# Kernel optimization log

Hardware: AMD Instinct MI355X
Metric: run time of the kernel (lower is better)

The kernel has to match this reference:

```python
import jax, jax.numpy as jnp
import numpy as np

N, C = 2, 256
GH0, GW0 = 40, 40
GH1, GW1 = 40, 40
STRIDE, TOPK = 2, 8
TEMP, THRESH, BORDER = 0.1, 0.2, 2
H0, W0 = GH0 * STRIDE, GW0 * STRIDE
H1, W1 = GH1 * STRIDE, GW1 * STRIDE
K4 = TOPK * STRIDE * STRIDE
# create_meshgrid(2,2) flattened: entries (x, y) in row-major (y outer) order
GRID = jnp.array([[0, 0], [1, 0], [0, 1], [1, 1]], dtype=jnp.int32)


def map_indices(idx, size0, size1):
    # idx: (n, G0, topk) coarse indices into image1 coarse grid
    row = idx[..., None] // size1[1] * STRIDE + GRID[:, 1]
    col = idx[..., None] % size1[1] * STRIDE + GRID[:, 0]
    fine = row * (size1[1] * STRIDE) + col  # (n, G0, topk, 4)
    n = idx.shape[0]
    fine = fine.reshape(n, size0[0], 1, size0[1], 1, -1)
    fine = jnp.broadcast_to(fine, (n, size0[0], STRIDE, size0[1], STRIDE, fine.shape[-1]))
    return fine.reshape(n, size0[0] * size0[1] * STRIDE * STRIDE, -1)


def remove_border_one_side(idx, br, size):
    h, w = size
    pos = jnp.arange(h * w)
    r, c = pos // w, pos % w
    border = (r < br) | (r >= h - br) | (c < br) | (c >= w - br)
    return jnp.where(border[None, :], 0, idx)


def unpatchify(x, grid, stride):
    n, g, s2, c = x.shape
    gh, gw = grid
    x = x.reshape(n, gh, gw, stride, stride, c)
    x = jnp.transpose(x, (0, 5, 1, 3, 2, 4))
    return x.reshape(n, c, gh * stride, gw * stride)


def fused_heatmaps(x0, x1, a01, a10, ind0_f, ind1_f):
    s01 = jnp.einsum('ngqc,ngkc->ngqk', x0, a01) / C  # (n, G0, 4, K4)
    s10 = jnp.einsum('ngqc,ngkc->ngqk', x1, a10) / C
    h01 = jax.nn.softmax(s01 / TEMP, axis=-1)
    h10 = jax.nn.softmax(s10 / TEMP, axis=-1)
    h01 = h01.reshape(N, GH0, GW0, STRIDE, STRIDE, K4)
    h01 = jnp.transpose(h01, (0, 1, 3, 2, 4, 5)).reshape(N, H0 * W0, K4)
    h10 = h10.reshape(N, GH1, GW1, STRIDE, STRIDE, K4)
    h10 = jnp.transpose(h10, (0, 5, 1, 3, 2, 4)).reshape(N, K4, H1 * W1)
    # dense scatter + gather mutual fusion (as in the torch code)
    b = jnp.arange(N)[:, None, None]
    l1 = jnp.arange(H1 * W1)[None, None, :]
    Z0 = jnp.zeros((N, H0 * W0, H1 * W1), h10.dtype).at[b, ind1_f, l1].set(h10)
    new_h01 = h01 * jnp.take_along_axis(Z0, ind0_f, axis=-1)
    l0 = jnp.arange(H0 * W0)[None, :, None]
    Z1 = jnp.zeros((N, H0 * W0, H1 * W1), h01.dtype).at[b, l0, ind0_f].set(h01)
    new_h10 = h10 * jnp.take_along_axis(Z1, ind1_f, axis=-2)
    return new_h01, new_h10


def coarse_matching(h01, h10, ind0_f, ind1_f):
    score = jnp.max(h01, axis=-1)                 # (n, L0)
    sub0 = jnp.argmax(h01, axis=-1)               # (n, L0)
    j_best = jnp.take_along_axis(ind0_f, sub0[..., None], axis=-1)[..., 0]
    sub1 = jnp.argmax(h10, axis=-2)               # (n, L1)
    i_best = jnp.take_along_axis(ind1_f, sub1[:, None, :], axis=-2)[:, 0, :]
    j_best = remove_border_one_side(j_best, BORDER, (H1, W1))
    i_best = remove_border_one_side(i_best, BORDER, (H0, W0))
    biproj = jnp.take_along_axis(i_best, j_best, axis=-1)
    mask = biproj == jnp.arange(H0 * W0)[None, :]
    mask = mask.at[:, 0].set(False)
    mask = mask & (score > THRESH)
    scores = jnp.where(mask, score, 0.0)
    return mask, j_best, scores


def setup_inputs() -> dict:
    key = jax.random.key(0)
    ks = jax.random.split(key, 6)
    return {
        'x0': jax.random.normal(ks[0], (N, GH0 * GW0, 4, C), jnp.float32),
        'x1': jax.random.normal(ks[1], (N, GH1 * GW1, 4, C), jnp.float32),
        'attended0_to_1': jax.random.normal(ks[2], (N, GH0 * GW0, K4, C), jnp.float32),
        'attended1_to_0': jax.random.normal(ks[3], (N, GH1 * GW1, K4, C), jnp.float32),
        'x0_prior': jax.random.normal(ks[4], (N, C, GH0, GW0), jnp.float32),
        'x1_prior': jax.random.normal(ks[5], (N, C, GH1, GW1), jnp.float32),
    }


def reference(x0, x1, attended0_to_1, attended1_to_0, x0_prior, x1_prior):
    p0 = x0_prior.reshape(N, C, GH0 * GW0)
    p1 = x1_prior.reshape(N, C, GH1 * GW1)
    sim = jnp.einsum('nci,ncj->nij', p0, p1) / C  # (n, G0, G1)
    _, i01 = jax.lax.top_k(sim, TOPK)                              # (n, G0, topk)
    _, i10 = jax.lax.top_k(jnp.swapaxes(sim, -2, -1), TOPK)        # (n, G1, topk)
    ind0_f = map_indices(i01, (GH0, GW0), (GH1, GW1))              # (n, L0, K4)
    ind1_f = jnp.swapaxes(map_indices(i10, (GH1, GW1), (GH0, GW0)), -2, -1)  # (n, K4, L1)
    h01, h10 = fused_heatmaps(x0, x1, attended0_to_1, attended1_to_0, ind0_f, ind1_f)
    mask, j_best, scores = coarse_matching(jax.lax.stop_gradient(h01), jax.lax.stop_gradient(h10), ind0_f, ind1_f)
    x0_8x = unpatchify(x0, (GH0, GW0), STRIDE)
    x1_8x = unpatchify(x1, (GH1, GW1), STRIDE)
    return h01, h10, scores, j_best, mask, x0_8x, x1_8x
```

## Files before the change

### kernel.cpp

```cpp
#include <hip/hip_runtime.h>


#define N_B   2
#define C_DIM 256
#define G0N   1600
#define GW    40
#define L0N   6400
#define W_F   80
#define TK    8

#define KC 32
__global__ __launch_bounds__(128) void k_sim(const float* __restrict__ p0,
                                             const float* __restrict__ p1,
                                             float* __restrict__ sim,
                                             float* __restrict__ simT) {
  const int n  = blockIdx.z;
  const int i0 = blockIdx.y * 64;
  const int j0 = blockIdx.x * 64;
  const float* A = p0 + (size_t)n * C_DIM * G0N;
  const float* B = p1 + (size_t)n * C_DIM * G0N;
  __shared__ float As[KC][64];
  __shared__ float Bs[KC][64];
  const int t  = threadIdx.x;
  const int tx = t & 15;
  const int ty = t >> 4;

  float4 acc[8];
#pragma unroll
  for (int ii = 0; ii < 8; ++ii) acc[ii] = make_float4(0.f, 0.f, 0.f, 0.f);

  for (int kc = 0; kc < C_DIM; kc += KC) {
#pragma unroll
    for (int u = 0; u < 4; ++u) {
      int f   = t + u * 128;
      int row = f >> 4;
      int c4  = (f & 15) * 4;
      *(float4*)&As[row][c4] = *(const float4*)(A + (size_t)(kc + row) * G0N + i0 + c4);
      *(float4*)&Bs[row][c4] = *(const float4*)(B + (size_t)(kc + row) * G0N + j0 + c4);
    }
    __syncthreads();
#pragma unroll
    for (int k = 0; k < KC; ++k) {
      __attribute__((aligned(16))) float a[8];
      *(float4*)&a[0] = *(const float4*)&As[k][ty * 8];
      *(float4*)&a[4] = *(const float4*)&As[k][ty * 8 + 4];
      float4 bv = *(const float4*)&Bs[k][tx * 4];
#pragma unroll
      for (int ii = 0; ii < 8; ++ii) {
        acc[ii].x += a[ii] * bv.x;
        acc[ii].y += a[ii] * bv.y;
        acc[ii].z += a[ii] * bv.z;
        acc[ii].w += a[ii] * bv.w;
      }
    }
    __syncthreads();
  }

  float* simn  = sim  + (size_t)n * G0N * G0N;
  float* simTn = simT + (size_t)n * G0N * G0N;
  const int ib = i0 + ty * 8;
  const int jb = j0 + tx * 4;
  const float* accf = (const float*)acc;
#pragma unroll
  for (int ii = 0; ii < 8; ++ii)
    *(float4*)(simn + (size_t)(ib + ii) * G0N + jb) = acc[ii];
#pragma unroll
  for (int jj = 0; jj < 4; ++jj) {
    float4 lo = make_float4(accf[0 * 4 + jj], accf[1 * 4 + jj], accf[2 * 4 + jj], accf[3 * 4 + jj]);
    float4 hi = make_float4(accf[4 * 4 + jj], accf[5 * 4 + jj], accf[6 * 4 + jj], accf[7 * 4 + jj]);
    *(float4*)(simTn + (size_t)(jb + jj) * G0N + ib)     = lo;
    *(float4*)(simTn + (size_t)(jb + jj) * G0N + ib + 4) = hi;
  }
}

__global__ __launch_bounds__(256) void k_topk(const float* __restrict__ sim,
                                              const float* __restrict__ simT,
                                              int* __restrict__ i01,
                                              int* __restrict__ i10) {
  int wid  = (blockIdx.x * 256 + threadIdx.x) >> 6;
  int lane = threadIdx.x & 63;
  int dir  = wid / (N_B * G0N);
  int r    = wid - dir * (N_B * G0N);
  const float* row = (dir ? simT : sim) + (size_t)r * G0N;
  int* out = (dir ? i10 : i01) + r * TK;

  float v[25];
#pragma unroll
  for (int tt = 0; tt < 25; ++tt) v[tt] = row[lane + 64 * tt];

#pragma unroll 1
  for (int k = 0; k < TK; ++k) {
    float best = -3.4e38f; int bidx = 0x7fffffff;
#pragma unroll
    for (int tt = 0; tt < 25; ++tt) {
      if (v[tt] > best) { best = v[tt]; bidx = lane + 64 * tt; }
    }
#pragma unroll
    for (int off = 1; off < 64; off <<= 1) {
      float ov = __shfl_xor(best, off);
      int   oi = __shfl_xor(bidx, off);
      if (ov > best || (ov == best && oi < bidx)) { best = ov; bidx = oi; }
    }
    if (lane == 0) out[k] = bidx;
#pragma unroll
    for (int tt = 0; tt < 25; ++tt)
      if (lane + 64 * tt == bidx) v[tt] = -3.4e38f;
  }
}

__global__ __launch_bounds__(128) void k_heat(const float* __restrict__ x0,
                                              const float* __restrict__ a01,
                                              float* __restrict__ h01p,
                                              const float* __restrict__ x1,
                                              const float* __restrict__ a10,
                                              float* __restrict__ h10p) {
  int bid = blockIdx.x;
  const float* x   = x0;
  const float* att = a01;
  float*       hpre = h01p;
  int ng = bid;
  if (bid >= N_B * G0N) { x = x1; att = a10; hpre = h10p; ng = bid - N_B * G0N; }
  const float* xp = x   + (size_t)ng * 4  * C_DIM;
  const float* ap = att + (size_t)ng * 32 * C_DIM;
  __shared__ float xs[4 * C_DIM];
  __shared__ float as[32][260];
  const int t = threadIdx.x;
#pragma unroll
  for (int j = 0; j < 16; ++j) {
    int f = t + j * 128;
    float4 v = *(const float4*)(ap + (size_t)f * 4);
    *(float4*)&as[f >> 6][(f & 63) * 4] = v;
  }
#pragma unroll
  for (int j = 0; j < 2; ++j) {
    int f = t + j * 128;
    *(float4*)&xs[f * 4] = *(const float4*)(xp + (size_t)f * 4);
  }
  __syncthreads();
  const int k4 = t & 31, q = t >> 5;
  float acc = 0.f;
#pragma unroll
  for (int c4 = 0; c4 < 64; ++c4) {
    float4 a  = *(const float4*)&as[k4][c4 * 4];
    float4 xv = *(const float4*)&xs[q * C_DIM + c4 * 4];
    acc += a.x * xv.x + a.y * xv.y + a.z * xv.z + a.w * xv.w;
  }
  float l = (acc * (1.0f / 256.0f)) / 0.1f;
  float m = l;
#pragma unroll
  for (int off = 1; off < 32; off <<= 1) m = fmaxf(m, __shfl_xor(m, off));
  float e = expf(l - m);
  float s = e;
#pragma unroll
  for (int off = 1; off < 32; off <<= 1) s += __shfl_xor(s, off);
  hpre[(size_t)ng * 128 + q * 32 + k4] = e / s;
}

__global__ __launch_bounds__(256) void k_fuse01(const float* __restrict__ h01p,
                                                const float* __restrict__ h10p,
                                                const int* __restrict__ i01,
                                                const int* __restrict__ i10,
                                                float* __restrict__ h01_out,
                                                float* __restrict__ score_ws,
                                                int* __restrict__ jbest_ws,
                                                float* __restrict__ jbest_out) {
  int idx = blockIdx.x * 8 + (threadIdx.x >> 5);
  int k4  = threadIdx.x & 31;
  int n = idx / L0N, l0 = idx - n * L0N;
  int r0 = l0 / W_F, c0 = l0 - r0 * W_F;
  int g0 = (r0 >> 1) * GW + (c0 >> 1);
  int q0 = ((r0 & 1) << 1) | (c0 & 1);
  int k = k4 >> 2, g = k4 & 3;
  int jc = i01[(n * G0N + g0) * TK + k];
  const int* row10 = i10 + (n * G0N + jc) * TK;
  int kf = -1;
#pragma unroll
  for (int kp = 0; kp < 8; ++kp) if (row10[kp] == g0) kf = kp;
  float m = 0.f;
  if (kf >= 0) m = h10p[((n * G0N + jc) * 4 + g) * 32 + kf * 4 + q0];
  float h = h01p[((n * G0N + g0) * 4 + q0) * 32 + k4];
  float val = h * m;
  h01_out[(size_t)idx * 32 + k4] = val;

  float best = val; int bi = k4;
#pragma unroll
  for (int off = 1; off < 32; off <<= 1) {
    float ov = __shfl_xor(best, off);
    int   oi = __shfl_xor(bi, off);
    if (ov > best || (ov == best && oi < bi)) { best = ov; bi = oi; }
  }
  if (k4 == 0) {
    score_ws[idx] = best;
    int kB = bi >> 2, gB = bi & 3;
    int jcB = i01[(n * G0N + g0) * TK + kB];
    int jrow = jcB / GW;
    int jb = ((jrow * 2 + (gB >> 1)) * W_F) + (jcB - jrow * GW) * 2 + (gB & 1);
    if (r0 < 2 || r0 >= W_F - 2 || c0 < 2 || c0 >= W_F - 2) jb = 0;
    jbest_ws[idx]  = jb;
    jbest_out[idx] = (float)jb;
  }
}

__global__ __launch_bounds__(256) void k_fuse10(const float* __restrict__ h01p,
                                                const float* __restrict__ h10p,
                                                const int* __restrict__ i01,
                                                const int* __restrict__ i10,
                                                float* __restrict__ h10_out,
                                                int* __restrict__ ibest_ws) {
  int idx = blockIdx.x * 8 + (threadIdx.x >> 5);
  int k4  = threadIdx.x & 31;
  int n = idx / L0N, l1 = idx - n * L0N;
  int r1 = l1 / W_F, c1 = l1 - r1 * W_F;
  int g1 = (r1 >> 1) * GW + (c1 >> 1);
  int q1 = ((r1 & 1) << 1) | (c1 & 1);
  int k = k4 >> 2, g = k4 & 3;
  int ic = i10[(n * G0N + g1) * TK + k];
  const int* row01 = i01 + (n * G0N + ic) * TK;
  int kf = -1;
#pragma unroll
  for (int kp = 0; kp < 8; ++kp) if (row01[kp] == g1) kf = kp;
  float m = 0.f;
  if (kf >= 0) m = h01p[((n * G0N + ic) * 4 + g) * 32 + kf * 4 + q1];
  float h = h10p[((n * G0N + g1) * 4 + q1) * 32 + k4];
  float val = h * m;
  h10_out[((size_t)n * 32 + k4) * L0N + l1] = val;

  float best = val; int bi = k4;
#pragma unroll
  for (int off = 1; off < 32; off <<= 1) {
    float ov = __shfl_xor(best, off);
    int   oi = __shfl_xor(bi, off);
    if (ov > best || (ov == best && oi < bi)) { best = ov; bi = oi; }
  }
  if (k4 == 0) {
    int kB = bi >> 2, gB = bi & 3;
    int icB = i10[(n * G0N + g1) * TK + kB];
    int irow = icB / GW;
    int ib = ((irow * 2 + (gB >> 1)) * W_F) + (icB - irow * GW) * 2 + (gB & 1);
    if (r1 < 2 || r1 >= W_F - 2 || c1 < 2 || c1 >= W_F - 2) ib = 0;
    ibest_ws[idx] = ib;
  }
}

__global__ __launch_bounds__(256) void k_final(const float* __restrict__ score_ws,
                                               const int* __restrict__ jbest_ws,
                                               const int* __restrict__ ibest_ws,
                                               float* __restrict__ scores_out,
                                               float* __restrict__ mask_out) {
  int idx = blockIdx.x * 256 + threadIdx.x;
  if (idx >= N_B * L0N) return;
  int n = idx / L0N, l0 = idx - n * L0N;
  int jb = jbest_ws[idx];
  float sc = score_ws[idx];
  int biproj = ibest_ws[n * L0N + jb];
  bool mk = (biproj == l0) && (l0 != 0) && (sc > 0.2f);
  scores_out[idx] = mk ? sc : 0.f;
  mask_out[idx]   = mk ? 1.f : 0.f;
}

__global__ __launch_bounds__(256) void k_unpatch(const float* __restrict__ x0,
                                                 float* __restrict__ out0,
                                                 const float* __restrict__ x1,
                                                 float* __restrict__ out1) {
  __shared__ float tile[32][33];
  int z = blockIdx.z;
  const float* x = (z < 16) ? x0 : x1;
  float* out     = (z < 16) ? out0 : out1;
  int zz  = z & 15;
  int cc0 = blockIdx.x * 32;
  int r   = blockIdx.y;
  int n   = zz >> 3;
  int c0  = (zz & 7) * 32;
  int t = threadIdx.x;
  int sr = r & 1, ghr = r >> 1;
  int pos = t >> 5, cl = t & 31;
#pragma unroll
  for (int it = 0; it < 4; ++it) {
    int p = pos + it * 8;
    int cc = cc0 + p;
    if (cc < W_F) {
      int gg = ghr * GW + (cc >> 1);
      int qq = (sr << 1) | (cc & 1);
      tile[p][cl] = x[(((size_t)n * G0N + gg) * 4 + qq) * C_DIM + c0 + cl];
    }
  }
  __syncthreads();
  int co = t >> 5, p2 = t & 31;
#pragma unroll
  for (int it = 0; it < 4; ++it) {
    int c = c0 + co + it * 8;
    int cc = cc0 + p2;
    if (cc < W_F)
      out[(((size_t)n * C_DIM + c) * W_F + r) * W_F + cc] = tile[p2][co + it * 8];
  }
}

extern "C" void kernel_launch(void* const* d_in, const int* in_sizes, int n_in,
                              void* d_out, int out_size, void* d_ws, size_t ws_size,
                              hipStream_t stream) {
  const float* x0  = (const float*)d_in[0];
  const float* x1  = (const float*)d_in[1];
  const float* a01 = (const float*)d_in[2];
  const float* a10 = (const float*)d_in[3];
  const float* p0  = (const float*)d_in[4];
  const float* p1  = (const float*)d_in[5];
  float* out = (float*)d_out;

  float* ws       = (float*)d_ws;
  float* sim      = ws;
  float* simT     = ws + 5120000;
  int*   i01      = (int*)(ws + 10240000);
  int*   i10      = (int*)(ws + 10265600);
  float* h01p     = ws + 10291200;
  float* h10p     = ws + 10700800;
  float* score_ws = ws + 11110400;
  int*   jbest_ws = (int*)(ws + 11123200);
  int*   ibest_ws = (int*)(ws + 11136000);

  float* o_h01   = out;
  float* o_h10   = out + 409600;
  float* o_score = out + 819200;
  float* o_jbest = out + 832000;
  float* o_mask  = out + 844800;
  float* o_x08   = out + 857600;
  float* o_x18   = out + 4134400;

  k_sim<<<dim3(25, 25, 2), 128, 0, stream>>>(p0, p1, sim, simT);
  k_topk<<<1600, 256, 0, stream>>>(sim, simT, i01, i10);
  k_heat<<<6400, 128, 0, stream>>>(x0, a01, h01p, x1, a10, h10p);
  k_fuse01<<<1600, 256, 0, stream>>>(h01p, h10p, i01, i10, o_h01, score_ws, jbest_ws, o_jbest);
  k_fuse10<<<1600, 256, 0, stream>>>(h01p, h10p, i01, i10, o_h10, ibest_ws);
  k_final<<<50, 256, 0, stream>>>(score_ws, jbest_ws, ibest_ws, o_score, o_mask);
  k_unpatch<<<dim3(3, 80, 32), 256, 0, stream>>>(x0, o_x08, x1, o_x18);
}
```

Baseline: 344.4 us.

## Compute heatmap scores per wavefront from global memory, skipping shared-memory staging

The heatmap kernel now gives each 64-lane wavefront one coarse cell instead of one 128-thread block. It reads attention rows and the four query vectors directly from global memory, with each half-wave covering half of the channel dimension and a cross-half shuffle completing the dot products. Each lane computes all four query rows, so the shared-memory staging and the barrier are no longer needed. The cost is strided per-lane float4 loads, which coalesce less well, and the x vectors being reloaded by every lane through cache.

```diff
diff --git a/kernel.cpp b/kernel.cpp
--- a/kernel.cpp
+++ b/kernel.cpp
@@ -108,52 +108,72 @@
   }
 }
 
-__global__ __launch_bounds__(128) void k_heat(const float* __restrict__ x0,
+__global__ __launch_bounds__(256) void k_heat(const float* __restrict__ x0,
                                               const float* __restrict__ a01,
                                               float* __restrict__ h01p,
                                               const float* __restrict__ x1,
                                               const float* __restrict__ a10,
                                               float* __restrict__ h10p) {
-  int bid = blockIdx.x;
+  int wid  = blockIdx.x * 4 + (threadIdx.x >> 6);
+  int lane = threadIdx.x & 63;
+  int k4   = lane & 31;
+  int cs   = lane >> 5;
   const float* x   = x0;
   const float* att = a01;
-  float*       hpre = h01p;
-  int ng = bid;
-  if (bid >= N_B * G0N) { x = x1; att = a10; hpre = h10p; ng = bid - N_B * G0N; }
-  const float* xp = x   + (size_t)ng * 4  * C_DIM;
-  const float* ap = att + (size_t)ng * 32 * C_DIM;
-  __shared__ float xs[4 * C_DIM];
-  __shared__ float as[32][260];
-  const int t = threadIdx.x;
-#pragma unroll
-  for (int j = 0; j < 16; ++j) {
-    int f = t + j * 128;
-    float4 v = *(const float4*)(ap + (size_t)f * 4);
-    *(float4*)&as[f >> 6][(f & 63) * 4] = v;
-  }
-#pragma unroll
-  for (int j = 0; j < 2; ++j) {
-    int f = t + j * 128;
-    *(float4*)&xs[f * 4] = *(const float4*)(xp + (size_t)f * 4);
-  }
-  __syncthreads();
-  const int k4 = t & 31, q = t >> 5;
-  float acc = 0.f;
-#pragma unroll
-  for (int c4 = 0; c4 < 64; ++c4) {
-    float4 a  = *(const float4*)&as[k4][c4 * 4];
-    float4 xv = *(const float4*)&xs[q * C_DIM + c4 * 4];
-    acc += a.x * xv.x + a.y * xv.y + a.z * xv.z + a.w * xv.w;
-  }
-  float l = (acc * (1.0f / 256.0f)) / 0.1f;
-  float m = l;
-#pragma unroll
-  for (int off = 1; off < 32; off <<= 1) m = fmaxf(m, __shfl_xor(m, off));
-  float e = expf(l - m);
-  float s = e;
-#pragma unroll
-  for (int off = 1; off < 32; off <<= 1) s += __shfl_xor(s, off);
-  hpre[(size_t)ng * 128 + q * 32 + k4] = e / s;
+  float*      hpre = h01p;
+  int ng = wid;
+  if (wid >= N_B * G0N) { x = x1; att = a10; hpre = h10p; ng = wid - N_B * G0N; }
+  const float* ar = att + ((size_t)ng * 32 + k4) * C_DIM + cs * 128;
+  const float* xr = x   + (size_t)ng * 4 * C_DIM + cs * 128;
+
+  float acc0 = 0.f, acc1 = 0.f, acc2 = 0.f, acc3 = 0.f;
+#pragma unroll 8
+  for (int it = 0; it < 32; ++it) {
+    float4 av  = *(const float4*)(ar + it * 4);
+    float4 xv0 = *(const float4*)(xr + 0 * C_DIM + it * 4);
+    float4 xv1 = *(const float4*)(xr + 1 * C_DIM + it * 4);
+    float4 xv2 = *(const float4*)(xr + 2 * C_DIM + it * 4);
+    float4 xv3 = *(const float4*)(xr + 3 * C_DIM + it * 4);
+    acc0 += av.x * xv0.x + av.y * xv0.y + av.z * xv0.z + av.w * xv0.w;
+    acc1 += av.x * xv1.x + av.y * xv1.y + av.z * xv1.z + av.w * xv1.w;
+    acc2 += av.x * xv2.x + av.y * xv2.y + av.z * xv2.z + av.w * xv2.w;
+    acc3 += av.x * xv3.x + av.y * xv3.y + av.z * xv3.z + av.w * xv3.w;
+  }
+  acc0 += __shfl_xor(acc0, 32);
+  acc1 += __shfl_xor(acc1, 32);
+  acc2 += __shfl_xor(acc2, 32);
+  acc3 += __shfl_xor(acc3, 32);
+
+  float l0 = (acc0 * (1.0f / 256.0f)) / 0.1f;
+  float l1 = (acc1 * (1.0f / 256.0f)) / 0.1f;
+  float l2 = (acc2 * (1.0f / 256.0f)) / 0.1f;
+  float l3 = (acc3 * (1.0f / 256.0f)) / 0.1f;
+
+  float m0 = l0, m1 = l1, m2 = l2, m3 = l3;
+#pragma unroll
+  for (int off = 1; off < 32; off <<= 1) {
+    m0 = fmaxf(m0, __shfl_xor(m0, off));
+    m1 = fmaxf(m1, __shfl_xor(m1, off));
+    m2 = fmaxf(m2, __shfl_xor(m2, off));
+    m3 = fmaxf(m3, __shfl_xor(m3, off));
+  }
+  float e0 = expf(l0 - m0), e1 = expf(l1 - m1), e2 = expf(l2 - m2), e3 = expf(l3 - m3);
+  float s0 = e0, s1 = e1, s2 = e2, s3 = e3;
+#pragma unroll
+  for (int off = 1; off < 32; off <<= 1) {
+    s0 += __shfl_xor(s0, off);
+    s1 += __shfl_xor(s1, off);
+    s2 += __shfl_xor(s2, off);
+    s3 += __shfl_xor(s3, off);
+  }
+  float* op = hpre + (size_t)ng * 128 + k4;
+  if (cs == 0) {
+    op[0]  = e0 / s0;
+    op[32] = e1 / s1;
+  } else {
+    op[64] = e2 / s2;
+    op[96] = e3 / s3;
+  }
 }
 
 __global__ __launch_bounds__(256) void k_fuse01(const float* __restrict__ h01p,
@@ -327,7 +347,7 @@
 
   k_sim<<<dim3(25, 25, 2), 128, 0, stream>>>(p0, p1, sim, simT);
   k_topk<<<1600, 256, 0, stream>>>(sim, simT, i01, i10);
-  k_heat<<<6400, 128, 0, stream>>>(x0, a01, h01p, x1, a10, h10p);
+  k_heat<<<1600, 256, 0, stream>>>(x0, a01, h01p, x1, a10, h10p);
   k_fuse01<<<1600, 256, 0, stream>>>(h01p, h10p, i01, i10, o_h01, score_ws, jbest_ws, o_jbest);
   k_fuse10<<<1600, 256, 0, stream>>>(h01p, h10p, i01, i10, o_h10, ibest_ws);
   k_final<<<50, 256, 0, stream>>>(score_ws, jbest_ws, ibest_ws, o_score, o_mask);
```

New measurement: 374.3 us. 1.09x slower.
